# Kernel tuning notes

Hardware: AMD Instinct MI355X
Metric: run time of the kernel (lower is better)

## Reference

```python
import jax, jax.numpy as jnp
import numpy as np

IN_DIM, COND_DIM, OUT_DIM = 256, 256, 128
B, LQ, LK = 4, 4096, 4096


def setup_inputs() -> dict:
    key = jax.random.key(0)
    ks = jax.random.split(key, 8)
    s_in = 1.0 / np.sqrt(IN_DIM)
    s_c = 1.0 / np.sqrt(COND_DIM)
    return {
        "x": jax.random.normal(ks[0], (B, LQ, IN_DIM), dtype=jnp.float32),
        "cond": jax.random.normal(ks[1], (B, LK, COND_DIM), dtype=jnp.float32),
        "Wq": jax.random.uniform(ks[2], (IN_DIM, OUT_DIM), jnp.float32, -s_in, s_in),
        "bq": jax.random.uniform(ks[3], (OUT_DIM,), jnp.float32, -s_in, s_in),
        "Wk": jax.random.uniform(ks[4], (COND_DIM, OUT_DIM), jnp.float32, -s_c, s_c),
        "bk": jax.random.uniform(ks[5], (OUT_DIM,), jnp.float32, -s_c, s_c),
        "Wv": jax.random.uniform(ks[6], (COND_DIM, OUT_DIM), jnp.float32, -s_c, s_c),
        "bv": jax.random.uniform(ks[7], (OUT_DIM,), jnp.float32, -s_c, s_c),
    }


def reference(x, cond, Wq, bq, Wk, bk, Wv, bv):
    # q: [B, Lq, D], k/v: [B, Lk, D]
    q = jnp.einsum("bqi,id->bqd", x, Wq) + bq
    k = jnp.einsum("bkc,cd->bkd", cond, Wk) + bk
    v = jnp.einsum("bkc,cd->bkd", cond, Wv) + bv
    # NOTE: original uses UNscaled dot product (no 1/sqrt(d)).
    scores = jnp.einsum("bqd,bkd->bqk", q, k)  # [B, Lq, Lk]
    attn = jax.nn.softmax(scores, axis=-1)
    return jnp.einsum("bqk,bkd->bqd", attn, v)  # [B, Lq, D]
```

## Files before the change

### kernel.cpp

```cpp
#include <hip/hip_runtime.h>
#include <hip/hip_bf16.h>


typedef __attribute__((ext_vector_type(8))) short short8;
typedef __attribute__((ext_vector_type(8))) unsigned short ushort8;
typedef __attribute__((ext_vector_type(4))) unsigned short us4;
typedef __attribute__((ext_vector_type(4))) float f32x4;
typedef __attribute__((ext_vector_type(16))) float f32x16;
typedef __attribute__((ext_vector_type(4))) unsigned int u32x4;
typedef __bf16 bf16x8 __attribute__((ext_vector_type(8)));

constexpr int BATCH  = 4;
constexpr int SEQLEN = 4096;
constexpr int DIN    = 256;
constexpr int DOUT   = 128;
constexpr int ROWS   = BATCH * SEQLEN;
constexpr float LOG2E = 1.4426950408889634f;

static __device__ __forceinline__ unsigned short bf16_rn(float f) {
  unsigned int u = __builtin_bit_cast(unsigned int, f);
  unsigned int r = u + 0x7FFFu + ((u >> 16) & 1u);
  return (unsigned short)(r >> 16);
}
static __device__ __forceinline__ float bf16_f32(unsigned short h) {
  return __builtin_bit_cast(float, (unsigned int)h << 16);
}
static __device__ __forceinline__ float exp2n(float x) {
  return __builtin_amdgcn_exp2f(x);
}

static __device__ __forceinline__ f32x4 mfma_bf16(short8 a, short8 b, f32x4 c) {
  return __builtin_amdgcn_mfma_f32_16x16x32_bf16(
      __builtin_bit_cast(bf16x8, a), __builtin_bit_cast(bf16x8, b), c, 0, 0, 0);
}
static __device__ __forceinline__ f32x16 mfma32(short8 a, short8 b, f32x16 c) {
  return __builtin_amdgcn_mfma_f32_32x32x16_bf16(
      __builtin_bit_cast(bf16x8, a), __builtin_bit_cast(bf16x8, b), c, 0, 0, 0);
}

static __device__ __forceinline__ unsigned int cvt_pk(float lo, float hi) {
  unsigned int r;
  asm("v_cvt_pk_bf16_f32 %0, %1, %2" : "=v"(r) : "v"(lo), "v"(hi));
  return r;
}
static __device__ __forceinline__ void permswap(unsigned int& a, unsigned int& b) {
  asm("v_permlane32_swap_b32 %0, %1" : "+v"(a), "+v"(b));
}

static __device__ __forceinline__ int swz128(int a) {
  return a ^ (((a >> 7) & 7) << 4);
}
static __device__ __forceinline__ int swzK(int a) {
  return a ^ (((a >> 8) & 15) << 4);
}


__global__ __launch_bounds__(256) void proj_kernel(
    const float* __restrict__ x, const float* __restrict__ cond,
    const float* __restrict__ Wq, const float* __restrict__ bq,
    const float* __restrict__ Wk, const float* __restrict__ bk,
    const float* __restrict__ Wv, const float* __restrict__ bv,
    unsigned short* __restrict__ qb, unsigned short* __restrict__ kb,
    unsigned short* __restrict__ vt)
{
  const int which = blockIdx.y;
  const float* __restrict__ src  = (which == 0) ? x  : cond;
  const float* __restrict__ W    = (which == 0) ? Wq : (which == 1 ? Wk : Wv);
  const float* __restrict__ bias = (which == 0) ? bq : (which == 1 ? bk : bv);
  const int r0 = blockIdx.x * 64;

  __shared__ __align__(16) char lds[32768];
  char* const AhB = lds;
  char* const AlB = lds + 8192;
  char* const WtB = lds + 16384;

  const int tid  = threadIdx.x;
  const int wv   = tid >> 6;
  const int lane = tid & 63;
  const int g    = lane >> 4;
  const int c    = lane & 15;

  f32x4 acc[8];
  #pragma unroll
  for (int cf = 0; cf < 8; ++cf) acc[cf] = (f32x4){0.f, 0.f, 0.f, 0.f};

  for (int kt = 0; kt < 4; ++kt) {
    #pragma unroll
    for (int i = 0; i < 4; ++i) {
      const int idx = tid + i * 256;
      const int row = idx >> 4, f4 = idx & 15;
      const float4 a4 =
          *(const float4*)(src + (size_t)(r0 + row) * DIN + kt * 64 + f4 * 4);
      us4 hi, lo;
      const float av[4] = {a4.x, a4.y, a4.z, a4.w};
      #pragma unroll
      for (int e = 0; e < 4; ++e) {
        hi[e] = bf16_rn(av[e]);
        lo[e] = bf16_rn(av[e] - bf16_f32(hi[e]));
      }
      const int off = swz128(row * 128 + f4 * 8);
      *(us4*)(AhB + off) = hi;
      *(us4*)(AlB + off) = lo;
    }
    {
      const int col = tid & 127, half = tid >> 7;
      #pragma unroll
      for (int j = 0; j < 4; ++j) {
        const int k0 = half * 32 + j * 8;
        ushort8 wb;
        #pragma unroll
        for (int e = 0; e < 8; ++e)
          wb[e] = bf16_rn(W[(size_t)(kt * 64 + k0 + e) * DOUT + col]);
        *(ushort8*)(WtB + swz128(col * 128 + k0 * 2)) = wb;
      }
    }
    __syncthreads();

    #pragma unroll
    for (int ks = 0; ks < 2; ++ks) {
      const int aoff = (wv * 16 + c) * 128 + ks * 64 + g * 16;
      const short8 ah = *(const short8*)(AhB + swz128(aoff));
      const short8 al = *(const short8*)(AlB + swz128(aoff));
      #pragma unroll
      for (int cf = 0; cf < 8; ++cf) {
        const short8 wb =
            *(const short8*)(WtB + swz128((cf * 16 + c) * 128 + ks * 64 + g * 16));
        acc[cf] = mfma_bf16(ah, wb, acc[cf]);
        acc[cf] = mfma_bf16(al, wb, acc[cf]);
      }
    }
    __syncthreads();
  }

  if (which == 0) {
    #pragma unroll
    for (int cf = 0; cf < 8; ++cf) {
      const float bb = bias[cf * 16 + c];
      #pragma unroll
      for (int r = 0; r < 4; ++r)
        qb[(size_t)(r0 + wv * 16 + g * 4 + r) * DOUT + cf * 16 + c] =
            bf16_rn((acc[cf][r] + bb) * LOG2E);
    }
  } else if (which == 1) {
    char* const Ktile = lds;
    #pragma unroll
    for (int cf = 0; cf < 8; ++cf) {
      const float bb = bias[cf * 16 + c];
      #pragma unroll
      for (int r = 0; r < 4; ++r) {
        const int row = wv * 16 + g * 4 + r;
        *(unsigned short*)(Ktile + swzK(row * 256 + (cf * 16 + c) * 2)) =
            bf16_rn(acc[cf][r] + bb);
      }
    }
    __syncthreads();
    const int b2     = r0 >> 12;
    const int kblkG0 = (r0 & 4095) >> 5;
    #pragma unroll
    for (int j = 0; j < 4; ++j) {
      const int i    = tid + j * 256;
      const int kblk = i >> 9;
      const int rem  = i & 511;
      const int f    = rem >> 6;
      const int ln   = rem & 63;
      const int row  = kblk * 32 + (ln & 31);
      const int colb = f * 32 + (ln >> 5) * 16;
      const ushort8 v = *(const ushort8*)(Ktile + swzK(row * 256 + colb));
      *(ushort8*)((char*)kb +
          (((size_t)(b2 * 128 + kblkG0 + kblk) * 8 + f) * 64 + ln) * 16) = v;
    }
  } else {
    const int keybase = r0 + wv * 16 + g * 4;
    const int b2   = keybase >> 12;
    const int kblk = (keybase & 4095) >> 5;
    const int kk   = (keybase >> 4) & 1;
    const int h    = (keybase >> 3) & 1;
    const int e0   = keybase & 7;
    #pragma unroll
    for (int cf = 0; cf < 8; ++cf) {
      const float bb = bias[cf * 16 + c];
      const int col  = cf * 16 + c;
      const int dblk = col >> 5, l31 = col & 31;
      us4 pk;
      #pragma unroll
      for (int r = 0; r < 4; ++r) pk[r] = bf16_rn(acc[cf][r] + bb);
      *(us4*)(vt + (((((size_t)b2 * 128 + kblk) * 4 + dblk) * 2 + kk) * 64 +
                    h * 32 + l31) * 8 + e0) = pk;
    }
  }
}

constexpr int NSPLIT = 4;
constexpr int QBLK   = 32;
constexpr int KVBLK  = 32;
constexpr int ITERS  = SEQLEN / NSPLIT / KVBLK;

__global__ __launch_bounds__(256)
__attribute__((amdgpu_waves_per_eu(2, 2)))
void attn_kernel(
    const unsigned short* __restrict__ qb,
    const unsigned short* __restrict__ kb,
    const unsigned short* __restrict__ vt,
    float* __restrict__ out)
{
  __shared__ __align__(16) float cmb[2][32][132];
  __shared__ float Ml[NSPLIT][32][2];

  const int bid = ((blockIdx.x & 7) << 6) | (blockIdx.x >> 3);
  const int qt  = bid & 127;
  const int b   = bid >> 7;
  const int tid = threadIdx.x;
  const int split = tid >> 6;
  const int lane  = tid & 63;
  const int ql = lane & 31;
  const int h  = lane >> 5;

  const int q0 = qt * QBLK;

  short8 qf[8];
  {
    const char* qp = (const char*)(qb + (size_t)(b * SEQLEN + q0 + ql) * DOUT) + h * 16;
    #pragma unroll
    for (int f = 0; f < 8; ++f) qf[f] = *(const short8*)(qp + f * 32);
  }

  const int kblk0 = split * (SEQLEN / NSPLIT / 32);
  const char* kfb = (const char*)kb + ((size_t)b * 128 + kblk0) * 8192 + lane * 16;
  const char* vfb = (const char*)vt + ((size_t)b * 128 + kblk0) * 8192 + lane * 16;

  f32x16 acc[4];
  #pragma unroll
  for (int d = 0; d < 4; ++d)
    #pragma unroll
    for (int r = 0; r < 16; ++r) acc[d][r] = 0.f;
  float mc = -1e30f, lc = 0.f;

  short8 kfA[8], kfB[8], vf[4][2];
  #pragma unroll
  for (int f = 0; f < 8; ++f) kfA[f] = *(const short8*)(kfb + f * 1024);
  #pragma unroll
  for (int f = 0; f < 8; ++f) kfB[f] = *(const short8*)(kfb + 8192 + f * 1024);
  kfb += 16384;
  #pragma unroll
  for (int d = 0; d < 4; ++d)
    #pragma unroll
    for (int kk = 0; kk < 2; ++kk)
      vf[d][kk] = *(const short8*)(vfb + (d * 2 + kk) * 1024);
  __builtin_amdgcn_sched_barrier(0);

  auto body = [&](short8 (&kf)[8], int t) {
    f32x16 s0, s1;
    #pragma unroll
    for (int r = 0; r < 16; ++r) { s0[r] = 0.f; s1[r] = 0.f; }
    __builtin_amdgcn_s_setprio(1);
    #pragma unroll
    for (int f = 0; f < 4; ++f) s0 = mfma32(kf[f], qf[f], s0);
    #pragma unroll
    for (int f = 0; f < 4; ++f) s1 = mfma32(kf[f + 4], qf[f + 4], s1);
    __builtin_amdgcn_s_setprio(0);

    if (t + 2 < ITERS) {
      #pragma unroll
      for (int f = 0; f < 8; ++f) kf[f] = *(const short8*)(kfb + f * 1024);
      kfb += 8192;
    }
    __builtin_amdgcn_sched_barrier(0);

    float s[16];
    #pragma unroll
    for (int r = 0; r < 16; ++r) s[r] = s0[r] + s1[r];

    float m01 = fmaxf(fmaxf(s[0],  s[1]),  s[2]);
    float m02 = fmaxf(fmaxf(s[3],  s[4]),  s[5]);
    float m03 = fmaxf(fmaxf(s[6],  s[7]),  s[8]);
    float m04 = fmaxf(fmaxf(s[9],  s[10]), s[11]);
    float m05 = fmaxf(fmaxf(s[12], s[13]), s[14]);
    float m11 = fmaxf(fmaxf(m01, m02), m03);
    float m12 = fmaxf(fmaxf(m04, m05), s[15]);
    float tm  = fmaxf(m11, m12);
    if (!__all(tm <= mc + 11.f)) {
      float tr = fmaxf(tm, __shfl_xor(tm, 32));
      const float mnew  = fmaxf(mc, tr);
      const float sc    = exp2n(mc - mnew);
      mc = mnew;
      lc *= sc;
      #pragma unroll
      for (int d = 0; d < 4; ++d)
        #pragma unroll
        for (int r = 0; r < 16; ++r) acc[d][r] *= sc;
    }
    float p[16];
    #pragma unroll
    for (int r = 0; r < 16; ++r) p[r] = exp2n(s[r] - mc);
    float a0 = (p[0]+p[1]) + (p[2]+p[3]);
    float a1 = (p[4]+p[5]) + (p[6]+p[7]);
    float a2 = (p[8]+p[9]) + (p[10]+p[11]);
    float a3 = (p[12]+p[13]) + (p[14]+p[15]);
    lc += (a0 + a1) + (a2 + a3);

    short8 pfrag[2];
    #pragma unroll
    for (int kk = 0; kk < 2; ++kk) {
      unsigned int A  = cvt_pk(p[kk * 8 + 0], p[kk * 8 + 1]);
      unsigned int Bv = cvt_pk(p[kk * 8 + 2], p[kk * 8 + 3]);
      unsigned int C  = cvt_pk(p[kk * 8 + 4], p[kk * 8 + 5]);
      unsigned int Dv = cvt_pk(p[kk * 8 + 6], p[kk * 8 + 7]);
      permswap(A, C);
      permswap(Bv, Dv);
      const u32x4 w = {A, Bv, C, Dv};
      pfrag[kk] = __builtin_bit_cast(short8, w);
    }

    __builtin_amdgcn_s_setprio(1);
    #pragma unroll
    for (int d = 0; d < 4; ++d)
      #pragma unroll
      for (int kk = 0; kk < 2; ++kk)
        acc[d] = mfma32(vf[d][kk], pfrag[kk], acc[d]);
    __builtin_amdgcn_s_setprio(0);

    if (t + 1 < ITERS) {
      vfb += 8192;
      #pragma unroll
      for (int d = 0; d < 4; ++d)
        #pragma unroll
        for (int kk = 0; kk < 2; ++kk)
          vf[d][kk] = *(const short8*)(vfb + (d * 2 + kk) * 1024);
    }
    __builtin_amdgcn_sched_barrier(0);
  };

  for (int t = 0; t < ITERS; t += 2) {
    body(kfA, t);
    body(kfB, t + 1);
  }

  lc += __shfl_xor(lc, 32);
  if (lane < 32) { Ml[split][ql][0] = mc; Ml[split][ql][1] = lc; }
  __syncthreads();

  float mg = -1e30f, lsum = 0.f;
  #pragma unroll
  for (int s2 = 0; s2 < NSPLIT; ++s2) mg = fmaxf(mg, Ml[s2][ql][0]);
  #pragma unroll
  for (int s2 = 0; s2 < NSPLIT; ++s2)
    lsum += Ml[s2][ql][1] * exp2n(Ml[s2][ql][0] - mg);
  const float fac = exp2n(mc - mg);
  #pragma unroll
  for (int d = 0; d < 4; ++d)
    #pragma unroll
    for (int r = 0; r < 16; ++r) acc[d][r] *= fac;

  if (split & 1) {
    float* reg = &cmb[split >> 1][0][0];
    #pragma unroll
    for (int d = 0; d < 4; ++d)
      #pragma unroll
      for (int rr = 0; rr < 4; ++rr) {
        const f32x4 v = {acc[d][rr*4+0], acc[d][rr*4+1], acc[d][rr*4+2], acc[d][rr*4+3]};
        *(f32x4*)(reg + ql * 132 + d * 32 + rr * 8 + h * 4) = v;
      }
  }
  __syncthreads();
  if (!(split & 1)) {
    const float* reg = &cmb[split >> 1][0][0];
    #pragma unroll
    for (int d = 0; d < 4; ++d)
      #pragma unroll
      for (int rr = 0; rr < 4; ++rr) {
        const f32x4 v = *(const f32x4*)(reg + ql * 132 + d * 32 + rr * 8 + h * 4);
        acc[d][rr*4+0] += v.x; acc[d][rr*4+1] += v.y;
        acc[d][rr*4+2] += v.z; acc[d][rr*4+3] += v.w;
      }
  }
  __syncthreads();
  if (split == 2) {
    float* reg = &cmb[0][0][0];
    #pragma unroll
    for (int d = 0; d < 4; ++d)
      #pragma unroll
      for (int rr = 0; rr < 4; ++rr) {
        const f32x4 v = {acc[d][rr*4+0], acc[d][rr*4+1], acc[d][rr*4+2], acc[d][rr*4+3]};
        *(f32x4*)(reg + ql * 132 + d * 32 + rr * 8 + h * 4) = v;
      }
  }
  __syncthreads();
  if (split == 0) {
    const float* reg = &cmb[0][0][0];
    const float inv = 1.f / lsum;
    float* const op = out + (size_t)(b * SEQLEN + q0 + ql) * DOUT;
    #pragma unroll
    for (int d = 0; d < 4; ++d)
      #pragma unroll
      for (int rr = 0; rr < 4; ++rr) {
        const f32x4 v = *(const f32x4*)(reg + ql * 132 + d * 32 + rr * 8 + h * 4);
        f32x4 o;
        o.x = (acc[d][rr*4+0] + v.x) * inv;
        o.y = (acc[d][rr*4+1] + v.y) * inv;
        o.z = (acc[d][rr*4+2] + v.z) * inv;
        o.w = (acc[d][rr*4+3] + v.w) * inv;
        *(f32x4*)(op + d * 32 + rr * 8 + h * 4) = o;
      }
  }
}

extern "C" void kernel_launch(void* const* d_in, const int* in_sizes, int n_in,
                              void* d_out, int out_size, void* d_ws, size_t ws_size,
                              hipStream_t stream) {
  const float* x    = (const float*)d_in[0];
  const float* cond = (const float*)d_in[1];
  const float* Wq   = (const float*)d_in[2];
  const float* bq   = (const float*)d_in[3];
  const float* Wk   = (const float*)d_in[4];
  const float* bk   = (const float*)d_in[5];
  const float* Wv   = (const float*)d_in[6];
  const float* bv   = (const float*)d_in[7];
  float* out = (float*)d_out;

  unsigned short* qb = (unsigned short*)d_ws;
  unsigned short* kb = qb + (size_t)ROWS * DOUT;
  unsigned short* vt = kb + (size_t)ROWS * DOUT;

  proj_kernel<<<dim3(ROWS / 64, 3), 256, 0, stream>>>(
      x, cond, Wq, bq, Wk, bk, Wv, bv, qb, kb, vt);

  attn_kernel<<<dim3(BATCH * (SEQLEN / QBLK)), 256, 0, stream>>>(
      qb, kb, vt, out);
}
```

Before: 71.66 us.

## Share K/V tiles across two query subtiles via LDS with async global-to-LDS loads

Doubles the block to 512 threads covering 64 queries (two 32-query subtiles per KV split), so each K/V tile is fetched once into LDS with global_load_lds and read by both waves of a split instead of each wave loading from global into registers. Loads are double-buffered in LDS with explicit vmcnt waits and block barriers per iteration. This halves global/L2 K/V traffic but adds per-iteration barriers, LDS reads, and 128KB LDS use that limits occupancy to one block per CU.

```diff
diff --git a/kernel.cpp b/kernel.cpp
--- a/kernel.cpp
+++ b/kernel.cpp
@@ -45,6 +45,12 @@
 }
 static __device__ __forceinline__ void permswap(unsigned int& a, unsigned int& b) {
   asm("v_permlane32_swap_b32 %0, %1" : "+v"(a), "+v"(b));
+}
+
+static __device__ __forceinline__ void gl16(const void* g, void* l) {
+  __builtin_amdgcn_global_load_lds(
+      (const __attribute__((address_space(1))) unsigned int*)g,
+      (__attribute__((address_space(3))) unsigned int*)l, 16, 0, 0);
 }
 
 static __device__ __forceinline__ int swz128(int a) {
@@ -191,31 +197,32 @@
 }
 
 constexpr int NSPLIT = 4;
-constexpr int QBLK   = 32;
 constexpr int KVBLK  = 32;
 constexpr int ITERS  = SEQLEN / NSPLIT / KVBLK;
 
-__global__ __launch_bounds__(256)
-__attribute__((amdgpu_waves_per_eu(2, 2)))
-void attn_kernel(
+__global__ __launch_bounds__(512) void attn_kernel(
     const unsigned short* __restrict__ qb,
     const unsigned short* __restrict__ kb,
     const unsigned short* __restrict__ vt,
     float* __restrict__ out)
 {
-  __shared__ __align__(16) float cmb[2][32][132];
-  __shared__ float Ml[NSPLIT][32][2];
-
-  const int bid = ((blockIdx.x & 7) << 6) | (blockIdx.x >> 3);
-  const int qt  = bid & 127;
-  const int b   = bid >> 7;
-  const int tid = threadIdx.x;
-  const int split = tid >> 6;
+  __shared__ __align__(16) char smem[131072];
+
+  const int bid = ((blockIdx.x & 7) << 5) | (blockIdx.x >> 3);
+  const int qt  = bid & 63;
+  const int b   = bid >> 6;
+  const int tid   = threadIdx.x;
+  const int wid   = tid >> 6;
+  const int qsub  = wid & 1;
+  const int split = wid >> 1;
   const int lane  = tid & 63;
   const int ql = lane & 31;
   const int h  = lane >> 5;
 
-  const int q0 = qt * QBLK;
+  const int q0 = qt * 64 + qsub * 32;
+
+  char* const KtB = smem + split * 32768;
+  char* const VtB = smem + split * 32768 + 16384;
 
   short8 qf[8];
   {
@@ -224,9 +231,9 @@
     for (int f = 0; f < 8; ++f) qf[f] = *(const short8*)(qp + f * 32);
   }
 
-  const int kblk0 = split * (SEQLEN / NSPLIT / 32);
-  const char* kfb = (const char*)kb + ((size_t)b * 128 + kblk0) * 8192 + lane * 16;
-  const char* vfb = (const char*)vt + ((size_t)b * 128 + kblk0) * 8192 + lane * 16;
+  const int kblk0 = split * 32;
+  const char* const kg = (const char*)kb + ((size_t)b * 128 + kblk0) * 8192 + lane * 16;
+  const char* const vg = (const char*)vt + ((size_t)b * 128 + kblk0) * 8192 + lane * 16;
 
   f32x16 acc[4];
   #pragma unroll
@@ -235,20 +242,49 @@
     for (int r = 0; r < 16; ++r) acc[d][r] = 0.f;
   float mc = -1e30f, lc = 0.f;
 
-  short8 kfA[8], kfB[8], vf[4][2];
-  #pragma unroll
-  for (int f = 0; f < 8; ++f) kfA[f] = *(const short8*)(kfb + f * 1024);
-  #pragma unroll
-  for (int f = 0; f < 8; ++f) kfB[f] = *(const short8*)(kfb + 8192 + f * 1024);
-  kfb += 16384;
-  #pragma unroll
-  for (int d = 0; d < 4; ++d)
-    #pragma unroll
-    for (int kk = 0; kk < 2; ++kk)
-      vf[d][kk] = *(const short8*)(vfb + (d * 2 + kk) * 1024);
+  if (qsub == 0) {
+    #pragma unroll
+    for (int f = 0; f < 8; ++f) gl16(kg + f * 1024, KtB + f * 1024);
+  } else {
+    #pragma unroll
+    for (int f = 0; f < 8; ++f) gl16(vg + f * 1024, VtB + f * 1024);
+  }
+  asm volatile("s_waitcnt vmcnt(0)" ::: "memory");
   __builtin_amdgcn_sched_barrier(0);
-
-  auto body = [&](short8 (&kf)[8], int t) {
+  __builtin_amdgcn_s_barrier();
+  __builtin_amdgcn_sched_barrier(0);
+
+  for (int t = 0; t < ITERS; ++t) {
+    const int cur = t & 1;
+
+    if (t + 1 < ITERS) {
+      const int nxt = cur ^ 1;
+      if (qsub == 0) {
+        const char* g = kg + (size_t)(t + 1) * 8192;
+        char* l = KtB + nxt * 8192;
+        #pragma unroll
+        for (int f = 0; f < 8; ++f) gl16(g + f * 1024, l + f * 1024);
+      } else {
+        const char* g = vg + (size_t)(t + 1) * 8192;
+        char* l = VtB + nxt * 8192;
+        #pragma unroll
+        for (int f = 0; f < 8; ++f) gl16(g + f * 1024, l + f * 1024);
+      }
+      asm volatile("s_waitcnt vmcnt(8)" ::: "memory");
+    } else {
+      asm volatile("s_waitcnt vmcnt(0)" ::: "memory");
+    }
+    __builtin_amdgcn_sched_barrier(0);
+    __builtin_amdgcn_s_barrier();
+    __builtin_amdgcn_sched_barrier(0);
+
+    const char* Kt = KtB + cur * 8192;
+    const char* Vt = VtB + cur * 8192;
+
+    short8 kf[8];
+    #pragma unroll
+    for (int f = 0; f < 8; ++f)
+      kf[f] = *(const short8*)(Kt + f * 1024 + lane * 16);
     f32x16 s0, s1;
     #pragma unroll
     for (int r = 0; r < 16; ++r) { s0[r] = 0.f; s1[r] = 0.f; }
@@ -258,13 +294,6 @@
     #pragma unroll
     for (int f = 0; f < 4; ++f) s1 = mfma32(kf[f + 4], qf[f + 4], s1);
     __builtin_amdgcn_s_setprio(0);
-
-    if (t + 2 < ITERS) {
-      #pragma unroll
-      for (int f = 0; f < 8; ++f) kf[f] = *(const short8*)(kfb + f * 1024);
-      kfb += 8192;
-    }
-    __builtin_amdgcn_sched_barrier(0);
 
     float s[16];
     #pragma unroll
@@ -315,44 +344,41 @@
     #pragma unroll
     for (int d = 0; d < 4; ++d)
       #pragma unroll
-      for (int kk = 0; kk < 2; ++kk)
-        acc[d] = mfma32(vf[d][kk], pfrag[kk], acc[d]);
+      for (int kk = 0; kk < 2; ++kk) {
+        const short8 vf = *(const short8*)(Vt + (d * 2 + kk) * 1024 + lane * 16);
+        acc[d] = mfma32(vf, pfrag[kk], acc[d]);
+      }
     __builtin_amdgcn_s_setprio(0);
 
-    if (t + 1 < ITERS) {
-      vfb += 8192;
-      #pragma unroll
-      for (int d = 0; d < 4; ++d)
-        #pragma unroll
-        for (int kk = 0; kk < 2; ++kk)
-          vf[d][kk] = *(const short8*)(vfb + (d * 2 + kk) * 1024);
-    }
     __builtin_amdgcn_sched_barrier(0);
-  };
-
-  for (int t = 0; t < ITERS; t += 2) {
-    body(kfA, t);
-    body(kfB, t + 1);
-  }
+    __builtin_amdgcn_s_barrier();
+    __builtin_amdgcn_sched_barrier(0);
+  }
+
+  __syncthreads();
+  float (*Ml)[NSPLIT][32][2] = (float(*)[NSPLIT][32][2])smem;
+  float* const cmbBase = (float*)(smem + 8192);
 
   lc += __shfl_xor(lc, 32);
-  if (lane < 32) { Ml[split][ql][0] = mc; Ml[split][ql][1] = lc; }
+  if (lane < 32) { Ml[qsub][split][ql][0] = mc; Ml[qsub][split][ql][1] = lc; }
   __syncthreads();
 
   float mg = -1e30f, lsum = 0.f;
   #pragma unroll
-  for (int s2 = 0; s2 < NSPLIT; ++s2) mg = fmaxf(mg, Ml[s2][ql][0]);
+  for (int s2 = 0; s2 < NSPLIT; ++s2) mg = fmaxf(mg, Ml[qsub][s2][ql][0]);
   #pragma unroll
   for (int s2 = 0; s2 < NSPLIT; ++s2)
-    lsum += Ml[s2][ql][1] * exp2n(Ml[s2][ql][0] - mg);
+    lsum += Ml[qsub][s2][ql][1] * exp2n(Ml[qsub][s2][ql][0] - mg);
   const float fac = exp2n(mc - mg);
   #pragma unroll
   for (int d = 0; d < 4; ++d)
     #pragma unroll
     for (int r = 0; r < 16; ++r) acc[d][r] *= fac;
 
-  if (split & 1) {
-    float* reg = &cmb[split >> 1][0][0];
+  float* const reg0 = cmbBase + (qsub * 2 + 0) * (32 * 132);
+  float* const reg1 = cmbBase + (qsub * 2 + 1) * (32 * 132);
+
+  auto writeReg = [&](float* reg) {
     #pragma unroll
     for (int d = 0; d < 4; ++d)
       #pragma unroll
@@ -360,10 +386,8 @@
         const f32x4 v = {acc[d][rr*4+0], acc[d][rr*4+1], acc[d][rr*4+2], acc[d][rr*4+3]};
         *(f32x4*)(reg + ql * 132 + d * 32 + rr * 8 + h * 4) = v;
       }
-  }
-  __syncthreads();
-  if (!(split & 1)) {
-    const float* reg = &cmb[split >> 1][0][0];
+  };
+  auto addReg = [&](const float* reg) {
     #pragma unroll
     for (int d = 0; d < 4; ++d)
       #pragma unroll
@@ -372,33 +396,27 @@
         acc[d][rr*4+0] += v.x; acc[d][rr*4+1] += v.y;
         acc[d][rr*4+2] += v.z; acc[d][rr*4+3] += v.w;
       }
-  }
+  };
+
+  if (split & 1) writeReg((split >> 1) ? reg1 : reg0);
   __syncthreads();
-  if (split == 2) {
-    float* reg = &cmb[0][0][0];
-    #pragma unroll
-    for (int d = 0; d < 4; ++d)
-      #pragma unroll
-      for (int rr = 0; rr < 4; ++rr) {
-        const f32x4 v = {acc[d][rr*4+0], acc[d][rr*4+1], acc[d][rr*4+2], acc[d][rr*4+3]};
-        *(f32x4*)(reg + ql * 132 + d * 32 + rr * 8 + h * 4) = v;
-      }
-  }
+  if (!(split & 1)) addReg((split >> 1) ? reg1 : reg0);
+  __syncthreads();
+  if (split == 2) writeReg(reg0);
   __syncthreads();
   if (split == 0) {
-    const float* reg = &cmb[0][0][0];
+    addReg(reg0);
     const float inv = 1.f / lsum;
     float* const op = out + (size_t)(b * SEQLEN + q0 + ql) * DOUT;
     #pragma unroll
     for (int d = 0; d < 4; ++d)
       #pragma unroll
       for (int rr = 0; rr < 4; ++rr) {
-        const f32x4 v = *(const f32x4*)(reg + ql * 132 + d * 32 + rr * 8 + h * 4);
         f32x4 o;
-        o.x = (acc[d][rr*4+0] + v.x) * inv;
-        o.y = (acc[d][rr*4+1] + v.y) * inv;
-        o.z = (acc[d][rr*4+2] + v.z) * inv;
-        o.w = (acc[d][rr*4+3] + v.w) * inv;
+        o.x = acc[d][rr*4+0] * inv;
+        o.y = acc[d][rr*4+1] * inv;
+        o.z = acc[d][rr*4+2] * inv;
+        o.w = acc[d][rr*4+3] * inv;
         *(f32x4*)(op + d * 32 + rr * 8 + h * 4) = o;
       }
   }
@@ -424,6 +442,6 @@
   proj_kernel<<<dim3(ROWS / 64, 3), 256, 0, stream>>>(
       x, cond, Wq, bq, Wk, bk, Wv, bv, qb, kb, vt);
 
-  attn_kernel<<<dim3(BATCH * (SEQLEN / QBLK)), 256, 0, stream>>>(
+  attn_kernel<<<dim3(BATCH * (SEQLEN / 64)), 512, 0, stream>>>(
       qb, kb, vt, out);
 }
```

Result: no change. 72.82 us (+1.6%).
